# Kernel optimization log

Measured on AMD Instinct MI355X. Metric: run time of the kernel, lower is better.

Reference implementation:

```python
import jax, jax.numpy as jnp
import numpy as np

ALPHA_R = 0.1  # leak rate of rate variable r
ALPHA_S = 0.2  # leak rate of synaptic current I

B, T, IN, H, OUT = 32, 2048, 256, 1024, 128


def setup_inputs() -> dict:
    key = jax.random.key(0)
    k1, k2, k3, k4 = jax.random.split(key, 4)
    x = jax.random.normal(k1, (B, T, IN), dtype=jnp.float32)
    # Orthogonal-ish init approximated by scaled gaussians (spectral radius ~1)
    Win = jax.random.normal(k2, (H, IN), dtype=jnp.float32) / np.sqrt(IN)
    Wrec = jax.random.normal(k3, (H, H), dtype=jnp.float32) / np.sqrt(H)
    Wout = jax.random.uniform(k4, (OUT, H), dtype=jnp.float32)
    return {"x": x, "Win": Win, "Wrec": Wrec, "Wout": Wout}


def reference(x, Win, Wrec, Wout):
    # x: [B, T, IN]. State kept batch-major [B, H] (torch code uses [H, B]; same math transposed).
    b = x.shape[0]
    h = Wrec.shape[0]
    WinT, WrecT, WoutT = Win.T, Wrec.T, Wout.T

    def step(carry, xt):
        I, r = carry
        I = (1.0 - ALPHA_S) * I + ALPHA_S * (r @ WrecT + xt @ WinT)
        # r_t = (1-a_r) r + a_r tanh(I_t)
        r = (1.0 - ALPHA_R) * r + ALPHA_R * jnp.tanh(I)
        return (I, r), r @ WoutT  # out_t: [B, OUT]

    init = (jnp.zeros((b, h), x.dtype), jnp.zeros((b, h), x.dtype))
    _, ys = jax.lax.scan(step, init, jnp.swapaxes(x, 0, 1))  # ys: [T, B, OUT]
    return jnp.swapaxes(ys, 0, 1)  # [B, T, OUT]
```

## Files before the change

### kernel.cpp

```cpp
#include <hip/hip_runtime.h>
#include <math.h>


#define T_STEPS 2048
#define B_SZ 32
#define IN_SZ 256
#define H_SZ 1024
#define OUT_SZ 128
#define WGS 256
#define NWG 256
#define PB_WORDS (B_SZ * (H_SZ / 2))
#define WS_WORDS (2 * PB_WORDS)

typedef unsigned int u32;
typedef u32 u32x4 __attribute__((ext_vector_type(4)));
typedef float f32x4 __attribute__((ext_vector_type(4)));
typedef short s16x8 __attribute__((ext_vector_type(8)));

__global__ void nrnn_init_ws(u32* __restrict__ ws) {
  const int i = blockIdx.x * blockDim.x + threadIdx.x;
  if (i < WS_WORDS) ws[i] = 0x00000001u;
}

__device__ __forceinline__ u32 bf16r(float x) {
  const u32 b = __float_as_uint(x);
  return (b + 0x7FFFu + ((b >> 16) & 1u)) >> 16;
}
__device__ __forceinline__ void st_sys_u32(u32* p, u32 v) {
  __hip_atomic_store(p, v, __ATOMIC_RELAXED, __HIP_MEMORY_SCOPE_SYSTEM);
}
__device__ __forceinline__ float tanh_fast(float x) {
  const float cx = fminf(fmaxf(x, -15.f), 15.f);
  const float e = __expf(2.f * cx);
  return (e - 1.f) * __builtin_amdgcn_rcpf(e + 1.f);
}

__global__ void __launch_bounds__(WGS, 1)
nrnn_main(const float* __restrict__ x, const float* __restrict__ Win,
          const float* __restrict__ Wrec, const float* __restrict__ Wout,
          float* __restrict__ out, float* __restrict__ ws) {
  const int tid = (int)threadIdx.x;
  const int hg  = tid >> 5;
  const int s   = tid & 31;
  const int wv  = tid >> 6;
  const int ln  = tid & 63;
  const int bg  = (int)blockIdx.x & 7;
  const int jb  = (int)blockIdx.x >> 3;

  u32* pbuf = (u32*)ws;
  const int b0 = bg * 4;

  __shared__ __align__(16) char r_lds[4 * 2048];
  __shared__ float wacc_lds[2][32][4];
  __shared__ float4 padlds[4800];

  if (__float_as_uint(x[0]) == 0x7F800001u) padlds[tid].x = 1.f;

  s16x8 wfrag[32];
  {
    const int g = (ln >> 4) & 3;
    const float* wp;
    if (wv < 2)       wp = Wrec + (size_t)(jb * 32 + wv * 16 + (ln & 15)) * H_SZ;
    else if (wv == 2) wp = Wout + (size_t)(jb * 4 + (ln & 3)) * H_SZ;
    else              wp = Wrec;
    #pragma unroll
    for (int st = 0; st < 32; ++st) {
      const int k0 = st * 32 + g * 8;
      const float4 c0 = *(const float4*)(wp + k0);
      const float4 c1 = *(const float4*)(wp + k0 + 4);
      s16x8 w;
      w[0] = (short)bf16r(c0.x); w[1] = (short)bf16r(c0.y);
      w[2] = (short)bf16r(c0.z); w[3] = (short)bf16r(c0.w);
      w[4] = (short)bf16r(c1.x); w[5] = (short)bf16r(c1.y);
      w[6] = (short)bf16r(c1.z); w[7] = (short)bf16r(c1.w);
      wfrag[st] = w;
    }
  }

  float4 wi4[4][2];
  #pragma unroll
  for (int hh = 0; hh < 4; ++hh) {
    const float* ip = Win + (size_t)(jb * 32 + hg * 4 + hh) * IN_SZ + s * 4;
    wi4[hh][0] = *(const float4*)(ip);
    wi4[hh][1] = *(const float4*)(ip + 128);
  }

  float Ist[4] = {0.f, 0.f, 0.f, 0.f};
  float rloc[4] = {0.f, 0.f, 0.f, 0.f};

  {
    float wacc[4][4];
    #pragma unroll
    for (int b = 0; b < 4; ++b)
      #pragma unroll
      for (int hh = 0; hh < 4; ++hh) wacc[b][hh] = 0.f;
    #pragma unroll
    for (int b = 0; b < 4; ++b) {
      const float* xp = x + ((size_t)(b0 + b) * T_STEPS) * IN_SZ + s * 4;
      const float4 x0 = *(const float4*)(xp);
      const float4 x1 = *(const float4*)(xp + 128);
      #pragma unroll
      for (int hh = 0; hh < 4; ++hh) {
        float4 w4 = wi4[hh][0];
        wacc[b][hh] = fmaf(w4.x, x0.x, wacc[b][hh]);
        wacc[b][hh] = fmaf(w4.y, x0.y, wacc[b][hh]);
        wacc[b][hh] = fmaf(w4.z, x0.z, wacc[b][hh]);
        wacc[b][hh] = fmaf(w4.w, x0.w, wacc[b][hh]);
        w4 = wi4[hh][1];
        wacc[b][hh] = fmaf(w4.x, x1.x, wacc[b][hh]);
        wacc[b][hh] = fmaf(w4.y, x1.y, wacc[b][hh]);
        wacc[b][hh] = fmaf(w4.z, x1.z, wacc[b][hh]);
        wacc[b][hh] = fmaf(w4.w, x1.w, wacc[b][hh]);
      }
    }
    #pragma unroll
    for (int m = 1; m <= 16; m <<= 1)
      #pragma unroll
      for (int b = 0; b < 4; ++b)
        #pragma unroll
        for (int hh = 0; hh < 4; ++hh)
          wacc[b][hh] += __shfl_xor(wacc[b][hh], m, 64);
    if (s < 16) wacc_lds[0][hg * 4 + (s & 3)][s >> 2] = wacc[s >> 2][s & 3];
  }

  auto poll_stage = [&](int tcur) {
    const u32 etag = (((u32)(tcur - 1)) >> 1) & 1u;
    const u32* gp = pbuf + (size_t)((tcur + 1) & 1) * PB_WORDS + (size_t)bg * 2048u;
    const u32* p0 = gp + 4 * tid;
    const u32* p1 = gp + 1024 + 4 * tid;
    u32x4 a0, a1;
    bool ok;
    do {
      asm volatile(
          "global_load_dwordx4 %0, %2, off sc0 sc1\n\t"
          "global_load_dwordx4 %1, %3, off sc0 sc1\n\t"
          "s_waitcnt vmcnt(0)"
          : "=&v"(a0), "=&v"(a1) : "v"(p0), "v"(p1) : "memory");
      u32 bad = 0;
      #pragma unroll
      for (int i = 0; i < 4; ++i) { bad |= a0[i] ^ etag; bad |= a1[i] ^ etag; }
      ok = ((bad & 1u) == 0u);
    } while (__any(!ok));
    const int bi0 = tid >> 7, bi1 = 2 + (tid >> 7);
    *(u32x4*)(r_lds + ((16 * tid) ^ ((bi0 & 3) << 4) ^ ((bi0 & 1) << 6))) = a0;
    *(u32x4*)(r_lds + ((4096 + 16 * tid) ^ ((bi1 & 3) << 4) ^ ((bi1 & 1) << 6))) = a1;
  };

  for (int t = 0; t < T_STEPS; ++t) {
    const int tt = (t + 1 < T_STEPS) ? (t + 1) : (T_STEPS - 1);
    float4 xv[4][2];
    #pragma unroll
    for (int b = 0; b < 4; ++b) {
      const float* xp = x + ((size_t)(b0 + b) * T_STEPS + (size_t)tt) * IN_SZ + s * 4;
      xv[b][0] = *(const float4*)(xp);
      xv[b][1] = *(const float4*)(xp + 128);
    }

    poll_stage(t);
    __syncthreads();

    f32x4 acc = {0.f, 0.f, 0.f, 0.f};
    if (wv <= 2) {
      const int beff = ln & 3;
      const int g16 = ((ln >> 4) & 3) * 16;
      const int bswz = ((beff & 3) << 4) | ((beff & 1) << 6);
      const char* rb = r_lds + beff * 2048;
      #pragma unroll
      for (int st = 0; st < 32; ++st) {
        const s16x8 bf = *(const s16x8*)(rb + ((st * 64 + g16) ^ bswz));
        acc = __builtin_amdgcn_mfma_f32_16x16x32_bf16(wfrag[st], bf, acc, 0, 0, 0);
      }
    }

    if (wv < 2 && (ln & 12) == 0) {
      const int b = ln & 3;
      const int g = ln >> 4;
      const int rbase = wv * 16 + g * 4;
      const u32 ptag = (((u32)t) >> 1) & 1u;
      u32 pk0, pk1;
      {
        float In0 = fmaf(0.2f, acc[0] + wacc_lds[t & 1][rbase + 0][b], 0.8f * Ist[0]);
        float In1 = fmaf(0.2f, acc[1] + wacc_lds[t & 1][rbase + 1][b], 0.8f * Ist[1]);
        float In2 = fmaf(0.2f, acc[2] + wacc_lds[t & 1][rbase + 2][b], 0.8f * Ist[2]);
        float In3 = fmaf(0.2f, acc[3] + wacc_lds[t & 1][rbase + 3][b], 0.8f * Ist[3]);
        Ist[0] = In0; Ist[1] = In1; Ist[2] = In2; Ist[3] = In3;
        rloc[0] = fmaf(0.1f, tanh_fast(In0), 0.9f * rloc[0]);
        rloc[1] = fmaf(0.1f, tanh_fast(In1), 0.9f * rloc[1]);
        rloc[2] = fmaf(0.1f, tanh_fast(In2), 0.9f * rloc[2]);
        rloc[3] = fmaf(0.1f, tanh_fast(In3), 0.9f * rloc[3]);
        pk0 = ((bf16r(rloc[1]) << 16) | (bf16r(rloc[0]) & 0xFFFFu));
        pk0 = (pk0 & ~1u) | ptag;
        pk1 = ((bf16r(rloc[3]) << 16) | (bf16r(rloc[2]) & 0xFFFFu));
        pk1 = (pk1 & ~1u) | ptag;
      }
      u32* pw = pbuf + (size_t)(t & 1) * PB_WORDS
                + (size_t)(b0 + b) * 512 + jb * 16 + wv * 8 + g * 2;
      st_sys_u32(pw, pk0);
      st_sys_u32(pw + 1, pk1);
    }

    if (wv == 2 && ln < 4 && t > 0) {
      #pragma unroll
      for (int reg = 0; reg < 4; ++reg)
        out[((size_t)(b0 + ln) * T_STEPS + (size_t)(t - 1)) * OUT_SZ + jb * 4 + reg] = acc[reg];
    }

    {
      float wacc[4][4];
      #pragma unroll
      for (int b = 0; b < 4; ++b)
        #pragma unroll
        for (int hh = 0; hh < 4; ++hh) wacc[b][hh] = 0.f;
      #pragma unroll
      for (int b = 0; b < 4; ++b) {
        const float4 x0 = xv[b][0];
        const float4 x1 = xv[b][1];
        #pragma unroll
        for (int hh = 0; hh < 4; ++hh) {
          float4 w4 = wi4[hh][0];
          wacc[b][hh] = fmaf(w4.x, x0.x, wacc[b][hh]);
          wacc[b][hh] = fmaf(w4.y, x0.y, wacc[b][hh]);
          wacc[b][hh] = fmaf(w4.z, x0.z, wacc[b][hh]);
          wacc[b][hh] = fmaf(w4.w, x0.w, wacc[b][hh]);
          w4 = wi4[hh][1];
          wacc[b][hh] = fmaf(w4.x, x1.x, wacc[b][hh]);
          wacc[b][hh] = fmaf(w4.y, x1.y, wacc[b][hh]);
          wacc[b][hh] = fmaf(w4.z, x1.z, wacc[b][hh]);
          wacc[b][hh] = fmaf(w4.w, x1.w, wacc[b][hh]);
        }
      }
      #pragma unroll
      for (int m = 1; m <= 16; m <<= 1)
        #pragma unroll
        for (int b = 0; b < 4; ++b)
          #pragma unroll
          for (int hh = 0; hh < 4; ++hh)
            wacc[b][hh] += __shfl_xor(wacc[b][hh], m, 64);
      if (s < 16)
        wacc_lds[(t + 1) & 1][hg * 4 + (s & 3)][s >> 2] = wacc[s >> 2][s & 3];
    }

    __syncthreads();
  }

  poll_stage(T_STEPS);
  __syncthreads();
  {
    f32x4 acc = {0.f, 0.f, 0.f, 0.f};
    if (wv == 2) {
      const int beff = ln & 3;
      const int g16 = ((ln >> 4) & 3) * 16;
      const int bswz = ((beff & 3) << 4) | ((beff & 1) << 6);
      const char* rb = r_lds + beff * 2048;
      #pragma unroll
      for (int st = 0; st < 32; ++st) {
        const s16x8 bf = *(const s16x8*)(rb + ((st * 64 + g16) ^ bswz));
        acc = __builtin_amdgcn_mfma_f32_16x16x32_bf16(wfrag[st], bf, acc, 0, 0, 0);
      }
      if (ln < 4) {
        #pragma unroll
        for (int reg = 0; reg < 4; ++reg)
          out[((size_t)(b0 + ln) * T_STEPS + (size_t)(T_STEPS - 1)) * OUT_SZ + jb * 4 + reg] = acc[reg];
      }
    }
  }
}

extern "C" void kernel_launch(void* const* d_in, const int* in_sizes, int n_in,
                              void* d_out, int out_size, void* d_ws, size_t ws_size,
                              hipStream_t stream) {
  const float* xp    = (const float*)d_in[0];
  const float* winp  = (const float*)d_in[1];
  const float* wrecp = (const float*)d_in[2];
  const float* woutp = (const float*)d_in[3];
  float* outp = (float*)d_out;
  float* wsp  = (float*)d_ws;

  nrnn_init_ws<<<(WS_WORDS + 255) / 256, 256, 0, stream>>>((u32*)d_ws);

  nrnn_main<<<dim3(NWG), dim3(WGS), 0, stream>>>(xp, winp, wrecp, woutp, outp, wsp);
}
```

Before: 6.093 ms.

## Assign workgroups by XCC and poll XCC-local fast buffer with system fallback

Each workgroup reads its hardware XCC ID and takes a rank from an atomic counter, so the 32 workgroups of a batch group all sit on the same XCC. The r state is now written twice: to a fast buffer with a plain store and to the slow buffer with a system-coherent store. Pollers first read the fast buffer with only sc0 and fall back to the coherent slow buffer if too many tries fail. r_lds is double-buffered by step parity, which allows dropping the trailing __syncthreads in each step. The aim is lower cross-workgroup exchange latency and one fewer barrier per step. The risks are the extra store, a stall if a given XCC does not get exactly 32 workgroups, and reliance on the dispatch pattern for correctness.

```diff
diff --git a/kernel.cpp b/kernel.cpp
--- a/kernel.cpp
+++ b/kernel.cpp
@@ -10,24 +10,25 @@
 #define WGS 256
 #define NWG 256
 #define PB_WORDS (B_SZ * (H_SZ / 2))
-#define WS_WORDS (2 * PB_WORDS)
+#define FAST_OFF (2 * PB_WORDS)
+#define CNT_OFF  (4 * PB_WORDS)
+#define WS_WORDS (4 * PB_WORDS + 128)
 
 typedef unsigned int u32;
+typedef u32 u32x2 __attribute__((ext_vector_type(2)));
 typedef u32 u32x4 __attribute__((ext_vector_type(4)));
 typedef float f32x4 __attribute__((ext_vector_type(4)));
 typedef short s16x8 __attribute__((ext_vector_type(8)));
 
 __global__ void nrnn_init_ws(u32* __restrict__ ws) {
   const int i = blockIdx.x * blockDim.x + threadIdx.x;
-  if (i < WS_WORDS) ws[i] = 0x00000001u;
+  if (i < CNT_OFF) ws[i] = 0x00000001u;
+  else if (i < WS_WORDS) ws[i] = 0u;
 }
 
 __device__ __forceinline__ u32 bf16r(float x) {
   const u32 b = __float_as_uint(x);
   return (b + 0x7FFFu + ((b >> 16) & 1u)) >> 16;
-}
-__device__ __forceinline__ void st_sys_u32(u32* p, u32 v) {
-  __hip_atomic_store(p, v, __ATOMIC_RELAXED, __HIP_MEMORY_SCOPE_SYSTEM);
 }
 __device__ __forceinline__ float tanh_fast(float x) {
   const float cx = fminf(fmaxf(x, -15.f), 15.f);
@@ -44,17 +45,28 @@
   const int s   = tid & 31;
   const int wv  = tid >> 6;
   const int ln  = tid & 63;
-  const int bg  = (int)blockIdx.x & 7;
-  const int jb  = (int)blockIdx.x >> 3;
-
-  u32* pbuf = (u32*)ws;
+
+  __shared__ __align__(16) char smem[102400];
+  char* r_lds = smem;
+  float (*wacc_lds)[32][4] = (float (*)[32][4])(smem + 16384);
+  __shared__ u32 s_role[2];
+
+  if (tid == 0) {
+    u32 xcc;
+    asm volatile("s_getreg_b32 %0, hwreg(HW_REG_XCC_ID)" : "=s"(xcc));
+    xcc &= 7u;
+    u32* xcnt = (u32*)ws + CNT_OFF;
+    const u32 rank = atomicAdd(&xcnt[xcc * 16], 1u);
+    s_role[0] = xcc;
+    s_role[1] = rank & 31u;
+  }
+  __syncthreads();
+  const int bg = (int)s_role[0];
+  const int jb = (int)s_role[1];
   const int b0 = bg * 4;
 
-  __shared__ __align__(16) char r_lds[4 * 2048];
-  __shared__ float wacc_lds[2][32][4];
-  __shared__ float4 padlds[4800];
-
-  if (__float_as_uint(x[0]) == 0x7F800001u) padlds[tid].x = 1.f;
+  u32* slowb = (u32*)ws;
+  u32* fastb = (u32*)ws + FAST_OFF;
 
   s16x8 wfrag[32];
   {
@@ -87,6 +99,7 @@
 
   float Ist[4] = {0.f, 0.f, 0.f, 0.f};
   float rloc[4] = {0.f, 0.f, 0.f, 0.f};
+  bool fastOK = true;
 
   {
     float wacc[4][4];
@@ -125,25 +138,47 @@
 
   auto poll_stage = [&](int tcur) {
     const u32 etag = (((u32)(tcur - 1)) >> 1) & 1u;
-    const u32* gp = pbuf + (size_t)((tcur + 1) & 1) * PB_WORDS + (size_t)bg * 2048u;
-    const u32* p0 = gp + 4 * tid;
-    const u32* p1 = gp + 1024 + 4 * tid;
+    const size_t boff = (size_t)((tcur + 1) & 1) * PB_WORDS + (size_t)bg * 2048u;
+    const u32* fp0 = fastb + boff + 4 * tid;
+    const u32* fp1 = fastb + boff + 1024 + 4 * tid;
+    const u32* sp0 = slowb + boff + 4 * tid;
+    const u32* sp1 = slowb + boff + 1024 + 4 * tid;
     u32x4 a0, a1;
-    bool ok;
-    do {
-      asm volatile(
-          "global_load_dwordx4 %0, %2, off sc0 sc1\n\t"
-          "global_load_dwordx4 %1, %3, off sc0 sc1\n\t"
-          "s_waitcnt vmcnt(0)"
-          : "=&v"(a0), "=&v"(a1) : "v"(p0), "v"(p1) : "memory");
-      u32 bad = 0;
-      #pragma unroll
-      for (int i = 0; i < 4; ++i) { bad |= a0[i] ^ etag; bad |= a1[i] ^ etag; }
-      ok = ((bad & 1u) == 0u);
-    } while (__any(!ok));
+    bool got = false;
+    if (fastOK) {
+      int tries = (tcur < 4) ? 256 : 16;
+      while (tries-- > 0) {
+        asm volatile(
+            "global_load_dwordx4 %0, %2, off sc0\n\t"
+            "global_load_dwordx4 %1, %3, off sc0\n\t"
+            "s_waitcnt vmcnt(0)"
+            : "=&v"(a0), "=&v"(a1) : "v"(fp0), "v"(fp1) : "memory");
+        u32 bad = 0;
+        #pragma unroll
+        for (int i = 0; i < 4; ++i) { bad |= a0[i] ^ etag; bad |= a1[i] ^ etag; }
+        const bool ok = ((bad & 1u) == 0u);
+        if (__all(ok)) { got = true; break; }
+      }
+      if (!got) fastOK = false;
+    }
+    if (!got) {
+      bool ok;
+      do {
+        asm volatile(
+            "global_load_dwordx4 %0, %2, off sc0 sc1\n\t"
+            "global_load_dwordx4 %1, %3, off sc0 sc1\n\t"
+            "s_waitcnt vmcnt(0)"
+            : "=&v"(a0), "=&v"(a1) : "v"(sp0), "v"(sp1) : "memory");
+        u32 bad = 0;
+        #pragma unroll
+        for (int i = 0; i < 4; ++i) { bad |= a0[i] ^ etag; bad |= a1[i] ^ etag; }
+        ok = ((bad & 1u) == 0u);
+      } while (__any(!ok));
+    }
+    char* dst = r_lds + (size_t)(tcur & 1) * 8192;
     const int bi0 = tid >> 7, bi1 = 2 + (tid >> 7);
-    *(u32x4*)(r_lds + ((16 * tid) ^ ((bi0 & 3) << 4) ^ ((bi0 & 1) << 6))) = a0;
-    *(u32x4*)(r_lds + ((4096 + 16 * tid) ^ ((bi1 & 3) << 4) ^ ((bi1 & 1) << 6))) = a1;
+    *(u32x4*)(dst + ((16 * tid) ^ ((bi0 & 3) << 4) ^ ((bi0 & 1) << 6))) = a0;
+    *(u32x4*)(dst + ((4096 + 16 * tid) ^ ((bi1 & 3) << 4) ^ ((bi1 & 1) << 6))) = a1;
   };
 
   for (int t = 0; t < T_STEPS; ++t) {
@@ -164,7 +199,7 @@
       const int beff = ln & 3;
       const int g16 = ((ln >> 4) & 3) * 16;
       const int bswz = ((beff & 3) << 4) | ((beff & 1) << 6);
-      const char* rb = r_lds + beff * 2048;
+      const char* rb = r_lds + (size_t)(t & 1) * 8192 + beff * 2048;
       #pragma unroll
       for (int st = 0; st < 32; ++st) {
         const s16x8 bf = *(const s16x8*)(rb + ((st * 64 + g16) ^ bswz));
@@ -177,26 +212,24 @@
       const int g = ln >> 4;
       const int rbase = wv * 16 + g * 4;
       const u32 ptag = (((u32)t) >> 1) & 1u;
-      u32 pk0, pk1;
-      {
-        float In0 = fmaf(0.2f, acc[0] + wacc_lds[t & 1][rbase + 0][b], 0.8f * Ist[0]);
-        float In1 = fmaf(0.2f, acc[1] + wacc_lds[t & 1][rbase + 1][b], 0.8f * Ist[1]);
-        float In2 = fmaf(0.2f, acc[2] + wacc_lds[t & 1][rbase + 2][b], 0.8f * Ist[2]);
-        float In3 = fmaf(0.2f, acc[3] + wacc_lds[t & 1][rbase + 3][b], 0.8f * Ist[3]);
-        Ist[0] = In0; Ist[1] = In1; Ist[2] = In2; Ist[3] = In3;
-        rloc[0] = fmaf(0.1f, tanh_fast(In0), 0.9f * rloc[0]);
-        rloc[1] = fmaf(0.1f, tanh_fast(In1), 0.9f * rloc[1]);
-        rloc[2] = fmaf(0.1f, tanh_fast(In2), 0.9f * rloc[2]);
-        rloc[3] = fmaf(0.1f, tanh_fast(In3), 0.9f * rloc[3]);
-        pk0 = ((bf16r(rloc[1]) << 16) | (bf16r(rloc[0]) & 0xFFFFu));
-        pk0 = (pk0 & ~1u) | ptag;
-        pk1 = ((bf16r(rloc[3]) << 16) | (bf16r(rloc[2]) & 0xFFFFu));
-        pk1 = (pk1 & ~1u) | ptag;
-      }
-      u32* pw = pbuf + (size_t)(t & 1) * PB_WORDS
-                + (size_t)(b0 + b) * 512 + jb * 16 + wv * 8 + g * 2;
-      st_sys_u32(pw, pk0);
-      st_sys_u32(pw + 1, pk1);
+      float In0 = fmaf(0.2f, acc[0] + wacc_lds[t & 1][rbase + 0][b], 0.8f * Ist[0]);
+      float In1 = fmaf(0.2f, acc[1] + wacc_lds[t & 1][rbase + 1][b], 0.8f * Ist[1]);
+      float In2 = fmaf(0.2f, acc[2] + wacc_lds[t & 1][rbase + 2][b], 0.8f * Ist[2]);
+      float In3 = fmaf(0.2f, acc[3] + wacc_lds[t & 1][rbase + 3][b], 0.8f * Ist[3]);
+      Ist[0] = In0; Ist[1] = In1; Ist[2] = In2; Ist[3] = In3;
+      rloc[0] = fmaf(0.1f, tanh_fast(In0), 0.9f * rloc[0]);
+      rloc[1] = fmaf(0.1f, tanh_fast(In1), 0.9f * rloc[1]);
+      rloc[2] = fmaf(0.1f, tanh_fast(In2), 0.9f * rloc[2]);
+      rloc[3] = fmaf(0.1f, tanh_fast(In3), 0.9f * rloc[3]);
+      u32x2 pk;
+      pk[0] = (((bf16r(rloc[1]) << 16) | (bf16r(rloc[0]) & 0xFFFFu)) & ~1u) | ptag;
+      pk[1] = (((bf16r(rloc[3]) << 16) | (bf16r(rloc[2]) & 0xFFFFu)) & ~1u) | ptag;
+      const size_t po = (size_t)(t & 1) * PB_WORDS
+                        + (size_t)(b0 + b) * 512 + jb * 16 + wv * 8 + g * 2;
+      u32* pwF = fastb + po;
+      u32* pwS = slowb + po;
+      asm volatile("global_store_dwordx2 %0, %1, off" :: "v"(pwF), "v"(pk) : "memory");
+      asm volatile("global_store_dwordx2 %0, %1, off sc0 sc1" :: "v"(pwS), "v"(pk) : "memory");
     }
 
     if (wv == 2 && ln < 4 && t > 0) {
@@ -239,8 +272,6 @@
       if (s < 16)
         wacc_lds[(t + 1) & 1][hg * 4 + (s & 3)][s >> 2] = wacc[s >> 2][s & 3];
     }
-
-    __syncthreads();
   }
 
   poll_stage(T_STEPS);
@@ -251,7 +282,7 @@
       const int beff = ln & 3;
       const int g16 = ((ln >> 4) & 3) * 16;
       const int bswz = ((beff & 3) << 4) | ((beff & 1) << 6);
-      const char* rb = r_lds + beff * 2048;
+      const char* rb = r_lds + (size_t)(T_STEPS & 1) * 8192 + beff * 2048;
       #pragma unroll
       for (int st = 0; st < 32; ++st) {
         const s16x8 bf = *(const s16x8*)(rb + ((st * 64 + g16) ^ bswz));
```

Result: slower. 7.006 ms (+15.0%).

## Split each workgroup's batch into two interleaved groups to overlap exchange latency

Applied to the files above, without the earlier changes.

Each workgroup now handles two independent groups of 2 batch rows instead of one group of 4 rows, and processes them in alternating phases. While one group's recurrent matmul and state update run, the cross-workgroup exchange load for the other group is already in flight. The goal is to hide the global-memory polling latency of the per-step grid-wide handoff. State exchange now uses a single dwordx2 store and prefetched dwordx4 loads, and the LDS padding trick that limited occupancy is removed. The cost is more barriers per step, and MFMA columns are half-used (2 of 4 batch lanes), which roughly doubles MFMA issue per useful output.

```diff
diff --git a/kernel.cpp b/kernel.cpp
--- a/kernel.cpp
+++ b/kernel.cpp
@@ -3,16 +3,16 @@
 
 
 #define T_STEPS 2048
-#define B_SZ 32
 #define IN_SZ 256
 #define H_SZ 1024
 #define OUT_SZ 128
 #define WGS 256
 #define NWG 256
-#define PB_WORDS (B_SZ * (H_SZ / 2))
+#define PB_WORDS 16384
 #define WS_WORDS (2 * PB_WORDS)
 
 typedef unsigned int u32;
+typedef u32 u32x2 __attribute__((ext_vector_type(2)));
 typedef u32 u32x4 __attribute__((ext_vector_type(4)));
 typedef float f32x4 __attribute__((ext_vector_type(4)));
 typedef short s16x8 __attribute__((ext_vector_type(8)));
@@ -22,18 +22,102 @@
   if (i < WS_WORDS) ws[i] = 0x00000001u;
 }
 
-__device__ __forceinline__ u32 bf16r(float x) {
-  const u32 b = __float_as_uint(x);
+__device__ __forceinline__ u32 bf16r(float v) {
+  const u32 b = __float_as_uint(v);
   return (b + 0x7FFFu + ((b >> 16) & 1u)) >> 16;
 }
-__device__ __forceinline__ void st_sys_u32(u32* p, u32 v) {
-  __hip_atomic_store(p, v, __ATOMIC_RELAXED, __HIP_MEMORY_SCOPE_SYSTEM);
-}
-__device__ __forceinline__ float tanh_fast(float x) {
-  const float cx = fminf(fmaxf(x, -15.f), 15.f);
+__device__ __forceinline__ float tanh_fast(float v) {
+  const float cx = fminf(fmaxf(v, -15.f), 15.f);
   const float e = __expf(2.f * cx);
   return (e - 1.f) * __builtin_amdgcn_rcpf(e + 1.f);
 }
+
+#define SWEEP_RETRY(dst, ptr, etg)                                            \
+  for (;;) {                                                                  \
+    u32 bad_ = 0;                                                             \
+    bad_ |= (dst)[0] ^ (etg); bad_ |= (dst)[1] ^ (etg);                       \
+    bad_ |= (dst)[2] ^ (etg); bad_ |= (dst)[3] ^ (etg);                       \
+    if (!__any(bad_ & 1u)) break;                                             \
+    asm volatile("global_load_dwordx4 %0, %1, off sc0 sc1\n\t"                \
+                 "s_waitcnt vmcnt(0)"                                         \
+                 : "=&v"(dst) : "v"(ptr) : "memory");                         \
+  }
+
+#define PHASE(GS, G, OGS, t, SWCUR, SWNXT, NXTG, NXTB, IST, RL, XVI, ISSG, ISST, XVC) \
+  do {                                                                        \
+    const u32 etag_ = (((u32)((t) - 1)) >> 1) & 1u;                           \
+    const u32* sp_ = pbuf + (size_t)(((t) + 1) & 1) * PB_WORDS                \
+                     + (size_t)(G) * 1024 + 4 * tid;                          \
+    asm volatile("s_waitcnt vmcnt(0)" : "+v"(SWCUR) :: "memory");             \
+    SWEEP_RETRY(SWCUR, sp_, etag_);                                           \
+    {                                                                         \
+      const int byte0_ = 16 * tid;                                            \
+      const int swz_ = ((byte0_ >> 11) & 1) << 6;                             \
+      *(u32x4*)(&r_lds[GS][(t) & 1][0] + (byte0_ ^ swz_)) = SWCUR;            \
+    }                                                                         \
+    __syncthreads();                                                          \
+    {                                                                         \
+      const int it_ = (ISST) < T_STEPS ? (ISST) : (T_STEPS - 1);              \
+      ldx((ISSG), it_, XVI);                                                  \
+    }                                                                         \
+    f32x4 acc_ = {0.f, 0.f, 0.f, 0.f};                                        \
+    if (wv <= 2) {                                                            \
+      const int beff_ = ln & 1;                                               \
+      const int g16_ = ((ln >> 4) & 3) * 16;                                  \
+      const char* rb_ = &r_lds[GS][(t) & 1][0] + beff_ * 2048;                \
+      _Pragma("unroll")                                                       \
+      for (int st_ = 0; st_ < 32; ++st_) {                                    \
+        const s16x8 bf_ =                                                     \
+            *(const s16x8*)(rb_ + ((st_ * 64 + g16_) ^ (beff_ << 6)));        \
+        acc_ = __builtin_amdgcn_mfma_f32_16x16x32_bf16(wfrag[st_], bf_,       \
+                                                       acc_, 0, 0, 0);        \
+      }                                                                       \
+    }                                                                         \
+    if (wv < 2 && (ln & 14) == 0) {                                           \
+      const int b_ = ln & 1, g4_ = ln >> 4;                                   \
+      const int rbase_ = wv * 16 + g4_ * 4;                                   \
+      const u32 ptag_ = (((u32)(t)) >> 1) & 1u;                               \
+      const float I0_ =                                                       \
+          fmaf(0.2f, acc_[0] + wacc_lds[GS][(t) & 1][rbase_ + 0][b_],         \
+               0.8f * IST[0]);                                                \
+      const float I1_ =                                                       \
+          fmaf(0.2f, acc_[1] + wacc_lds[GS][(t) & 1][rbase_ + 1][b_],         \
+               0.8f * IST[1]);                                                \
+      const float I2_ =                                                       \
+          fmaf(0.2f, acc_[2] + wacc_lds[GS][(t) & 1][rbase_ + 2][b_],         \
+               0.8f * IST[2]);                                                \
+      const float I3_ =                                                       \
+          fmaf(0.2f, acc_[3] + wacc_lds[GS][(t) & 1][rbase_ + 3][b_],         \
+               0.8f * IST[3]);                                                \
+      IST[0] = I0_; IST[1] = I1_; IST[2] = I2_; IST[3] = I3_;                 \
+      RL[0] = fmaf(0.1f, tanh_fast(I0_), 0.9f * RL[0]);                       \
+      RL[1] = fmaf(0.1f, tanh_fast(I1_), 0.9f * RL[1]);                       \
+      RL[2] = fmaf(0.1f, tanh_fast(I2_), 0.9f * RL[2]);                       \
+      RL[3] = fmaf(0.1f, tanh_fast(I3_), 0.9f * RL[3]);                       \
+      u32x2 pk_;                                                              \
+      pk_[0] = (((bf16r(RL[1]) << 16) | (bf16r(RL[0]) & 0xFFFFu)) & ~1u) |    \
+               ptag_;                                                         \
+      pk_[1] = (((bf16r(RL[3]) << 16) | (bf16r(RL[2]) & 0xFFFFu)) & ~1u) |    \
+               ptag_;                                                         \
+      u32* pw_ = pbuf + (size_t)((t) & 1) * PB_WORDS + (size_t)(G) * 1024 +   \
+                 b_ * 512 + (jb * 16 + wv * 8 + g4_ * 2);                     \
+      asm volatile("global_store_dwordx2 %0, %1, off sc0 sc1"                 \
+                   :: "v"(pw_), "v"(pk_) : "memory");                         \
+    }                                                                         \
+    if (wv == 2 && ln < 2 && (t) > 0) {                                       \
+      _Pragma("unroll")                                                       \
+      for (int r_ = 0; r_ < 4; ++r_)                                          \
+        out[((size_t)(2 * (G) + ln) * T_STEPS + (size_t)((t) - 1)) * OUT_SZ + \
+            jb * 4 + r_] = acc_[r_];                                          \
+    }                                                                         \
+    {                                                                         \
+      const u32* np_ = pbuf + (size_t)(NXTB) * PB_WORDS +                     \
+                       (size_t)(NXTG) * 1024 + 4 * tid;                       \
+      asm volatile("global_load_dwordx4 %0, %1, off sc0 sc1"                  \
+                   : "=v"(SWNXT) : "v"(np_) : "memory");                      \
+    }                                                                         \
+    winx(XVC, &wacc_lds[OGS][((t) + 1) & 1][0]);                              \
+  } while (0)
 
 __global__ void __launch_bounds__(WGS, 1)
 nrnn_main(const float* __restrict__ x, const float* __restrict__ Win,
@@ -44,17 +128,14 @@
   const int s   = tid & 31;
   const int wv  = tid >> 6;
   const int ln  = tid & 63;
-  const int bg  = (int)blockIdx.x & 7;
+  const int P   = (int)blockIdx.x & 7;
   const int jb  = (int)blockIdx.x >> 3;
+  const int gA = P, gB = P + 8;
 
   u32* pbuf = (u32*)ws;
-  const int b0 = bg * 4;
-
-  __shared__ __align__(16) char r_lds[4 * 2048];
-  __shared__ float wacc_lds[2][32][4];
-  __shared__ float4 padlds[4800];
-
-  if (__float_as_uint(x[0]) == 0x7F800001u) padlds[tid].x = 1.f;
+
+  __shared__ __align__(16) char r_lds[2][2][4096];
+  __shared__ float wacc_lds[2][2][32][2];
 
   s16x8 wfrag[32];
   {
@@ -85,183 +166,126 @@
     wi4[hh][1] = *(const float4*)(ip + 128);
   }
 
-  float Ist[4] = {0.f, 0.f, 0.f, 0.f};
-  float rloc[4] = {0.f, 0.f, 0.f, 0.f};
-
-  {
-    float wacc[4][4];
-    #pragma unroll
-    for (int b = 0; b < 4; ++b)
-      #pragma unroll
-      for (int hh = 0; hh < 4; ++hh) wacc[b][hh] = 0.f;
-    #pragma unroll
-    for (int b = 0; b < 4; ++b) {
-      const float* xp = x + ((size_t)(b0 + b) * T_STEPS) * IN_SZ + s * 4;
-      const float4 x0 = *(const float4*)(xp);
-      const float4 x1 = *(const float4*)(xp + 128);
+  auto ldx = [&](int G, int tt, float4 (&xv)[2][2]) {
+    #pragma unroll
+    for (int b2 = 0; b2 < 2; ++b2) {
+      const float* xp = x + ((size_t)(2 * G + b2) * T_STEPS + (size_t)tt) * IN_SZ + s * 4;
+      xv[b2][0] = *(const float4*)(xp);
+      xv[b2][1] = *(const float4*)(xp + 128);
+    }
+  };
+  auto winx = [&](const float4 (&xv)[2][2], float (*dst)[2]) {
+    float wa[2][4];
+    #pragma unroll
+    for (int b2 = 0; b2 < 2; ++b2)
+      #pragma unroll
+      for (int hh = 0; hh < 4; ++hh) wa[b2][hh] = 0.f;
+    #pragma unroll
+    for (int b2 = 0; b2 < 2; ++b2) {
+      const float4 x0 = xv[b2][0];
+      const float4 x1 = xv[b2][1];
       #pragma unroll
       for (int hh = 0; hh < 4; ++hh) {
         float4 w4 = wi4[hh][0];
-        wacc[b][hh] = fmaf(w4.x, x0.x, wacc[b][hh]);
-        wacc[b][hh] = fmaf(w4.y, x0.y, wacc[b][hh]);
-        wacc[b][hh] = fmaf(w4.z, x0.z, wacc[b][hh]);
-        wacc[b][hh] = fmaf(w4.w, x0.w, wacc[b][hh]);
+        wa[b2][hh] = fmaf(w4.x, x0.x, wa[b2][hh]);
+        wa[b2][hh] = fmaf(w4.y, x0.y, wa[b2][hh]);
+        wa[b2][hh] = fmaf(w4.z, x0.z, wa[b2][hh]);
+        wa[b2][hh] = fmaf(w4.w, x0.w, wa[b2][hh]);
         w4 = wi4[hh][1];
-        wacc[b][hh] = fmaf(w4.x, x1.x, wacc[b][hh]);
-        wacc[b][hh] = fmaf(w4.y, x1.y, wacc[b][hh]);
-        wacc[b][hh] = fmaf(w4.z, x1.z, wacc[b][hh]);
-        wacc[b][hh] = fmaf(w4.w, x1.w, wacc[b][hh]);
+        wa[b2][hh] = fmaf(w4.x, x1.x, wa[b2][hh]);
+        wa[b2][hh] = fmaf(w4.y, x1.y, wa[b2][hh]);
+        wa[b2][hh] = fmaf(w4.z, x1.z, wa[b2][hh]);
+        wa[b2][hh] = fmaf(w4.w, x1.w, wa[b2][hh]);
       }
     }
     #pragma unroll
     for (int m = 1; m <= 16; m <<= 1)
       #pragma unroll
-      for (int b = 0; b < 4; ++b)
+      for (int b2 = 0; b2 < 2; ++b2)
         #pragma unroll
         for (int hh = 0; hh < 4; ++hh)
-          wacc[b][hh] += __shfl_xor(wacc[b][hh], m, 64);
-    if (s < 16) wacc_lds[0][hg * 4 + (s & 3)][s >> 2] = wacc[s >> 2][s & 3];
-  }
-
-  auto poll_stage = [&](int tcur) {
-    const u32 etag = (((u32)(tcur - 1)) >> 1) & 1u;
-    const u32* gp = pbuf + (size_t)((tcur + 1) & 1) * PB_WORDS + (size_t)bg * 2048u;
-    const u32* p0 = gp + 4 * tid;
-    const u32* p1 = gp + 1024 + 4 * tid;
-    u32x4 a0, a1;
-    bool ok;
-    do {
-      asm volatile(
-          "global_load_dwordx4 %0, %2, off sc0 sc1\n\t"
-          "global_load_dwordx4 %1, %3, off sc0 sc1\n\t"
-          "s_waitcnt vmcnt(0)"
-          : "=&v"(a0), "=&v"(a1) : "v"(p0), "v"(p1) : "memory");
-      u32 bad = 0;
-      #pragma unroll
-      for (int i = 0; i < 4; ++i) { bad |= a0[i] ^ etag; bad |= a1[i] ^ etag; }
-      ok = ((bad & 1u) == 0u);
-    } while (__any(!ok));
-    const int bi0 = tid >> 7, bi1 = 2 + (tid >> 7);
-    *(u32x4*)(r_lds + ((16 * tid) ^ ((bi0 & 3) << 4) ^ ((bi0 & 1) << 6))) = a0;
-    *(u32x4*)(r_lds + ((4096 + 16 * tid) ^ ((bi1 & 3) << 4) ^ ((bi1 & 1) << 6))) = a1;
+          wa[b2][hh] += __shfl_xor(wa[b2][hh], m, 64);
+    if (s < 8) dst[hg * 4 + (s & 3)][s >> 2] = wa[s >> 2][s & 3];
   };
 
+  float IstA[4] = {0.f, 0.f, 0.f, 0.f}, rlA[4] = {0.f, 0.f, 0.f, 0.f};
+  float IstB[4] = {0.f, 0.f, 0.f, 0.f}, rlB[4] = {0.f, 0.f, 0.f, 0.f};
+
+  float4 xvA[2][2], xvB[2][2];
+  {
+    float4 x0A[2][2], x0B[2][2];
+    ldx(gA, 0, x0A);
+    ldx(gB, 0, x0B);
+    winx(x0A, &wacc_lds[0][0][0]);
+    winx(x0B, &wacc_lds[1][0][0]);
+  }
+  ldx(gB, 1, xvB);
+  u32x4 swA, swB;
+  {
+    const u32* p0 = pbuf + (size_t)PB_WORDS + (size_t)gA * 1024 + 4 * tid;
+    asm volatile("global_load_dwordx4 %0, %1, off sc0 sc1"
+                 : "=v"(swA) : "v"(p0) : "memory");
+  }
+  __syncthreads();
+
   for (int t = 0; t < T_STEPS; ++t) {
-    const int tt = (t + 1 < T_STEPS) ? (t + 1) : (T_STEPS - 1);
-    float4 xv[4][2];
-    #pragma unroll
-    for (int b = 0; b < 4; ++b) {
-      const float* xp = x + ((size_t)(b0 + b) * T_STEPS + (size_t)tt) * IN_SZ + s * 4;
-      xv[b][0] = *(const float4*)(xp);
-      xv[b][1] = *(const float4*)(xp + 128);
-    }
-
-    poll_stage(t);
-    __syncthreads();
-
+    PHASE(0, gA, 1, t, swA, swB, gB, (t + 1) & 1, IstA, rlA,
+          xvA, gA, t + 1, xvB);
+    PHASE(1, gB, 0, t, swB, swA, gA, t & 1, IstB, rlB,
+          xvB, gB, t + 2, xvA);
+  }
+
+  const u32 etagF = (((u32)(T_STEPS - 1)) >> 1) & 1u;
+  {
+    const u32* sp = pbuf + (size_t)PB_WORDS + (size_t)gA * 1024 + 4 * tid;
+    asm volatile("s_waitcnt vmcnt(0)" : "+v"(swA) :: "memory");
+    SWEEP_RETRY(swA, sp, etagF);
+    const int byte0 = 16 * tid;
+    *(u32x4*)(&r_lds[0][0][0] + (byte0 ^ (((byte0 >> 11) & 1) << 6))) = swA;
+  }
+  __syncthreads();
+  if (wv == 2) {
     f32x4 acc = {0.f, 0.f, 0.f, 0.f};
-    if (wv <= 2) {
-      const int beff = ln & 3;
-      const int g16 = ((ln >> 4) & 3) * 16;
-      const int bswz = ((beff & 3) << 4) | ((beff & 1) << 6);
-      const char* rb = r_lds + beff * 2048;
-      #pragma unroll
-      for (int st = 0; st < 32; ++st) {
-        const s16x8 bf = *(const s16x8*)(rb + ((st * 64 + g16) ^ bswz));
-        acc = __builtin_amdgcn_mfma_f32_16x16x32_bf16(wfrag[st], bf, acc, 0, 0, 0);
-      }
-    }
-
-    if (wv < 2 && (ln & 12) == 0) {
-      const int b = ln & 3;
-      const int g = ln >> 4;
-      const int rbase = wv * 16 + g * 4;
-      const u32 ptag = (((u32)t) >> 1) & 1u;
-      u32 pk0, pk1;
-      {
-        float In0 = fmaf(0.2f, acc[0] + wacc_lds[t & 1][rbase + 0][b], 0.8f * Ist[0]);
-        float In1 = fmaf(0.2f, acc[1] + wacc_lds[t & 1][rbase + 1][b], 0.8f * Ist[1]);
-        float In2 = fmaf(0.2f, acc[2] + wacc_lds[t & 1][rbase + 2][b], 0.8f * Ist[2]);
-        float In3 = fmaf(0.2f, acc[3] + wacc_lds[t & 1][rbase + 3][b], 0.8f * Ist[3]);
-        Ist[0] = In0; Ist[1] = In1; Ist[2] = In2; Ist[3] = In3;
-        rloc[0] = fmaf(0.1f, tanh_fast(In0), 0.9f * rloc[0]);
-        rloc[1] = fmaf(0.1f, tanh_fast(In1), 0.9f * rloc[1]);
-        rloc[2] = fmaf(0.1f, tanh_fast(In2), 0.9f * rloc[2]);
-        rloc[3] = fmaf(0.1f, tanh_fast(In3), 0.9f * rloc[3]);
-        pk0 = ((bf16r(rloc[1]) << 16) | (bf16r(rloc[0]) & 0xFFFFu));
-        pk0 = (pk0 & ~1u) | ptag;
-        pk1 = ((bf16r(rloc[3]) << 16) | (bf16r(rloc[2]) & 0xFFFFu));
-        pk1 = (pk1 & ~1u) | ptag;
-      }
-      u32* pw = pbuf + (size_t)(t & 1) * PB_WORDS
-                + (size_t)(b0 + b) * 512 + jb * 16 + wv * 8 + g * 2;
-      st_sys_u32(pw, pk0);
-      st_sys_u32(pw + 1, pk1);
-    }
-
-    if (wv == 2 && ln < 4 && t > 0) {
-      #pragma unroll
-      for (int reg = 0; reg < 4; ++reg)
-        out[((size_t)(b0 + ln) * T_STEPS + (size_t)(t - 1)) * OUT_SZ + jb * 4 + reg] = acc[reg];
-    }
-
-    {
-      float wacc[4][4];
-      #pragma unroll
-      for (int b = 0; b < 4; ++b)
-        #pragma unroll
-        for (int hh = 0; hh < 4; ++hh) wacc[b][hh] = 0.f;
-      #pragma unroll
-      for (int b = 0; b < 4; ++b) {
-        const float4 x0 = xv[b][0];
-        const float4 x1 = xv[b][1];
-        #pragma unroll
-        for (int hh = 0; hh < 4; ++hh) {
-          float4 w4 = wi4[hh][0];
-          wacc[b][hh] = fmaf(w4.x, x0.x, wacc[b][hh]);
-          wacc[b][hh] = fmaf(w4.y, x0.y, wacc[b][hh]);
-          wacc[b][hh] = fmaf(w4.z, x0.z, wacc[b][hh]);
-          wacc[b][hh] = fmaf(w4.w, x0.w, wacc[b][hh]);
-          w4 = wi4[hh][1];
-          wacc[b][hh] = fmaf(w4.x, x1.x, wacc[b][hh]);
-          wacc[b][hh] = fmaf(w4.y, x1.y, wacc[b][hh]);
-          wacc[b][hh] = fmaf(w4.z, x1.z, wacc[b][hh]);
-          wacc[b][hh] = fmaf(w4.w, x1.w, wacc[b][hh]);
-        }
-      }
-      #pragma unroll
-      for (int m = 1; m <= 16; m <<= 1)
-        #pragma unroll
-        for (int b = 0; b < 4; ++b)
-          #pragma unroll
-          for (int hh = 0; hh < 4; ++hh)
-            wacc[b][hh] += __shfl_xor(wacc[b][hh], m, 64);
-      if (s < 16)
-        wacc_lds[(t + 1) & 1][hg * 4 + (s & 3)][s >> 2] = wacc[s >> 2][s & 3];
-    }
-
-    __syncthreads();
-  }
-
-  poll_stage(T_STEPS);
+    const int beff = ln & 1;
+    const int g16 = ((ln >> 4) & 3) * 16;
+    const char* rb = &r_lds[0][0][0] + beff * 2048;
+    #pragma unroll
+    for (int st = 0; st < 32; ++st) {
+      const s16x8 bf = *(const s16x8*)(rb + ((st * 64 + g16) ^ (beff << 6)));
+      acc = __builtin_amdgcn_mfma_f32_16x16x32_bf16(wfrag[st], bf, acc, 0, 0, 0);
+    }
+    if (ln < 2) {
+      #pragma unroll
+      for (int r = 0; r < 4; ++r)
+        out[((size_t)(2 * gA + ln) * T_STEPS + (size_t)(T_STEPS - 1)) * OUT_SZ +
+            jb * 4 + r] = acc[r];
+    }
+  }
+  {
+    const u32* sp = pbuf + (size_t)PB_WORDS + (size_t)gB * 1024 + 4 * tid;
+    asm volatile("global_load_dwordx4 %0, %1, off sc0 sc1\n\t"
+                 "s_waitcnt vmcnt(0)"
+                 : "=&v"(swB) : "v"(sp) : "memory");
+    SWEEP_RETRY(swB, sp, etagF);
+    const int byte0 = 16 * tid;
+    *(u32x4*)(&r_lds[1][0][0] + (byte0 ^ (((byte0 >> 11) & 1) << 6))) = swB;
+  }
   __syncthreads();
-  {
+  if (wv == 2) {
     f32x4 acc = {0.f, 0.f, 0.f, 0.f};
-    if (wv == 2) {
-      const int beff = ln & 3;
-      const int g16 = ((ln >> 4) & 3) * 16;
-      const int bswz = ((beff & 3) << 4) | ((beff & 1) << 6);
-      const char* rb = r_lds + beff * 2048;
-      #pragma unroll
-      for (int st = 0; st < 32; ++st) {
-        const s16x8 bf = *(const s16x8*)(rb + ((st * 64 + g16) ^ bswz));
-        acc = __builtin_amdgcn_mfma_f32_16x16x32_bf16(wfrag[st], bf, acc, 0, 0, 0);
-      }
-      if (ln < 4) {
-        #pragma unroll
-        for (int reg = 0; reg < 4; ++reg)
-          out[((size_t)(b0 + ln) * T_STEPS + (size_t)(T_STEPS - 1)) * OUT_SZ + jb * 4 + reg] = acc[reg];
-      }
+    const int beff = ln & 1;
+    const int g16 = ((ln >> 4) & 3) * 16;
+    const char* rb = &r_lds[1][0][0] + beff * 2048;
+    #pragma unroll
+    for (int st = 0; st < 32; ++st) {
+      const s16x8 bf = *(const s16x8*)(rb + ((st * 64 + g16) ^ (beff << 6)));
+      acc = __builtin_amdgcn_mfma_f32_16x16x32_bf16(wfrag[st], bf, acc, 0, 0, 0);
+    }
+    if (ln < 2) {
+      #pragma unroll
+      for (int r = 0; r < 4; ++r)
+        out[((size_t)(2 * gB + ln) * T_STEPS + (size_t)(T_STEPS - 1)) * OUT_SZ +
+            jb * 4 + r] = acc[r];
     }
   }
 }
```

Result: slower. 7.924 ms (+30.1%).
